# Kernel optimization log

Hardware: AMD Instinct MI355X
Metric: run time of the kernel (lower is better)

The kernel has to match this reference:

```python
import jax, jax.numpy as jnp
import numpy as np

N = 100000
E = 3200000
D = 256
HOPS = 3  # K + 1


def setup_inputs() -> dict:
    key = jax.random.key(0)
    k1, k2, k3, k4, k5 = jax.random.split(key, 5)
    node_features = jax.random.normal(k1, (N, D), dtype=jnp.float32)
    # glorot-uniform-like scale for K+1 Dense kernels
    limit = np.sqrt(6.0 / (D + D)).astype(np.float32)
    W = jax.random.uniform(k2, (HOPS, D, D), dtype=jnp.float32, minval=-limit, maxval=limit)
    adj_vals = jax.random.uniform(k3, (HOPS, E), dtype=jnp.float32)
    adj_rows = jax.random.randint(k4, (HOPS, E), 0, N, dtype=jnp.int32)
    adj_cols = jax.random.randint(k5, (HOPS, E), 0, N, dtype=jnp.int32)
    return {"node_features": node_features, "W": W, "adj_vals": adj_vals,
            "adj_rows": adj_rows, "adj_cols": adj_cols}


def reference(node_features, W, adj_vals, adj_rows, adj_cols):
    """Faithful eval-mode forward: sum over hops of SpMM(A_hop, X @ W_hop), then ReLU.
    Dropout is identity at inference (training=False)."""
    n = node_features.shape[0]
    out = jnp.zeros((n, W.shape[-1]), dtype=node_features.dtype)
    for hop in range(W.shape[0]):  # small fixed K+1 loop, structurally distinct hops
        feats = node_features @ W[hop]                      # [N, out_dim]
        msgs = adj_vals[hop][:, None] * feats[adj_cols[hop]]  # gather + scale, [E, out_dim]
        out = out + jax.ops.segment_sum(msgs, adj_rows[hop], num_segments=n)
    return jax.nn.relu(out)
```

## Files before the change

### kernel.cpp

```cpp
#include <hip/hip_runtime.h>

#define D 256
#define MAXB 128
#define SR 1024
#define PCH 16384

typedef __attribute__((ext_vector_type(8))) short short8;
typedef __attribute__((ext_vector_type(4))) float f32x4;

__device__ __forceinline__ ushort f2b(float f) {
    unsigned u = __float_as_uint(f);
    u += 0x7fffu + ((u >> 16) & 1u);
    return (ushort)(u >> 16);
}
__device__ __forceinline__ float b2f(ushort h) {
    return __uint_as_float(((unsigned)h) << 16);
}
__device__ __forceinline__ long long ntload_ll(const void* p) {
    return __builtin_nontemporal_load((const long long*)p);
}

__global__ void xconv_kernel(const float* __restrict__ X, ushort* __restrict__ Xb, int total8) {
    int i = blockIdx.x * 256 + threadIdx.x;
    if (i >= total8) return;
    const float4 a = *(const float4*)(X + (size_t)i * 8);
    const float4 b = *(const float4*)(X + (size_t)i * 8 + 4);
    ushort o8[8] = {f2b(a.x), f2b(a.y), f2b(a.z), f2b(a.w),
                    f2b(b.x), f2b(b.y), f2b(b.z), f2b(b.w)};
    *(short8*)(Xb + (size_t)i * 8) = *(const short8*)o8;
}

__global__ void wconv_kernel(const float* __restrict__ W, ushort* __restrict__ WT, int total) {
    int idx = blockIdx.x * 256 + threadIdx.x;
    if (idx >= total) return;
    int h = idx >> 16;
    int c = (idx >> 8) & 255, k = idx & 255;
    WT[(h << 16) + c * 256 + k] = f2b(W[(h << 16) + k * 256 + c]);
}

__global__ __launch_bounds__(512) void bpart_kernel(const int* __restrict__ rows,
                                                    const int* __restrict__ cols,
                                                    const float* __restrict__ vals,
                                                    int2* __restrict__ raw,
                                                    int* __restrict__ runofs,
                                                    int e, int nbuk, int nch) {
    __shared__ int lh[MAXB];
    __shared__ int lcur[MAXB];
    int h = blockIdx.y, c = blockIdx.x;
    int c0 = c * PCH, c1 = min(c0 + PCH, e);
    if (c0 >= c1) return;
    const int*   rr = rows + (size_t)h * e;
    const int*   cc = cols + (size_t)h * e;
    const float* vv = vals + (size_t)h * e;
    int tid = threadIdx.x;
    for (int k = tid; k < nbuk; k += 512) { lh[k] = 0; lcur[k] = 0; }
    __syncthreads();
    for (int i = c0 + tid; i < c1; i += 512)
        atomicAdd(&lh[rr[i] >> 10], 1);
    __syncthreads();
    int* ro = runofs + (size_t)(h * nch + c) * (nbuk + 1);
    if (tid == 0) {
        int run = h * e + c0;
        for (int j = 0; j < nbuk; ++j) {
            ro[j] = run;
            int v = lh[j];
            lh[j] = run;
            run += v;
        }
        ro[nbuk] = h * e + c1;
    }
    __syncthreads();
    for (int i = c0 + tid; i < c1; i += 512) {
        int row = rr[i];
        int b = row >> 10;
        int p = lh[b] + atomicAdd(&lcur[b], 1);
        raw[p] = make_int2(cc[i] | ((row & 1023) << 17), __float_as_int(vv[i]));
    }
}

__global__ __launch_bounds__(1024) void bscan_kernel(const int* __restrict__ runofs,
                                                     int* __restrict__ gbase,
                                                     int nbuk, int nch, int nkeytot) {
    __shared__ int s[1024];
    int t = threadIdx.x;
    int sum = 0;
    if (t < nkeytot) {
        int h = t / nbuk, b = t % nbuk;
        for (int c = 0; c < nch; ++c) {
            const int* ro = runofs + (size_t)(h * nch + c) * (nbuk + 1) + b;
            sum += ro[1] - ro[0];
        }
    }
    s[t] = sum;
    __syncthreads();
    for (int off = 1; off < 1024; off <<= 1) {
        int x = (t >= off) ? s[t - off] : 0;
        __syncthreads();
        s[t] += x;
        __syncthreads();
    }
    if (t < nkeytot) gbase[t] = s[t] - sum;
    if (t == nkeytot - 1) gbase[nkeytot] = s[t];
}

__global__ __launch_bounds__(512) void bsort_kernel(const int* __restrict__ gbase,
                                                    const int* __restrict__ runofs,
                                                    const int2* __restrict__ raw,
                                                    int2* __restrict__ eg,
                                                    int* __restrict__ row_ptr,
                                                    int n, int nbuk, int nch) {
    __shared__ int hist[1024];
    __shared__ int ss[512];
    __shared__ int cur[1024];
    int key = blockIdx.x;
    int h = key / nbuk, b = key % nbuk;
    int s = gbase[key], t = gbase[key + 1];
    int tid = threadIdx.x;
    int w = tid >> 6, lane = tid & 63;
    hist[tid] = 0; hist[tid + 512] = 0;
    __syncthreads();
    for (int c = w; c < nch; c += 8) {
        const int* ro = runofs + (size_t)(h * nch + c) * (nbuk + 1) + b;
        int rs = ro[0], re = ro[1];
        for (int i = rs + lane; i < re; i += 64)
            atomicAdd(&hist[(((unsigned)raw[i].x) >> 17) & 1023], 1);
    }
    __syncthreads();
    int a = hist[2 * tid], c2 = hist[2 * tid + 1];
    int pair = a + c2;
    ss[tid] = pair;
    __syncthreads();
    for (int off = 1; off < 512; off <<= 1) {
        int x = (tid >= off) ? ss[tid - off] : 0;
        __syncthreads();
        ss[tid] += x;
        __syncthreads();
    }
    int excl = s + ss[tid] - pair;
    cur[2 * tid] = excl;
    cur[2 * tid + 1] = excl + a;
    int* rp = row_ptr + (size_t)h * (n + 1);
    int grow = b * SR + 2 * tid;
    if (grow < n)     rp[grow]     = excl;
    if (grow + 1 < n) rp[grow + 1] = excl + a;
    if (tid == 0 && b == nbuk - 1) rp[n] = t;
    __syncthreads();
    for (int c = w; c < nch; c += 8) {
        const int* ro = runofs + (size_t)(h * nch + c) * (nbuk + 1) + b;
        int rs = ro[0], re = ro[1];
        for (int i = rs + lane; i < re; i += 64) {
            int2 ev = raw[i];
            int j = (((unsigned)ev.x) >> 17) & 1023;
            int p = atomicAdd(&cur[j], 1);
            eg[p] = ev;
        }
    }
}

__global__ __launch_bounds__(256) void spmmX_kernel(const int* __restrict__ row_ptr,
                                                    const int2* __restrict__ eg,
                                                    const ushort* __restrict__ Xb,
                                                    ushort* __restrict__ Y, int n,
                                                    size_t rpStride, size_t yStride, int half) {
    const int* rp = row_ptr + blockIdx.y * rpStride;
    ushort* Yh = Y + blockIdx.y * yStride;
    int w = threadIdx.x >> 6, lane = threadIdx.x & 63;
    int r = blockIdx.x * 4 + w;
    if (r >= n) return;
    int g = lane >> 4, l4 = lane & 15;
    int doff = half * 128 + l4 * 8;
    const ushort* xb = Xb + doff;
    int e0 = rp[r], e1 = rp[r + 1];
    float acc[8] = {};

    int i0 = e0 + g;
    long long d_cur = (i0 < e1) ? ntload_ll(eg + i0) : 0;
    int c_cur = ((int)(unsigned)d_cur) & 0x1FFFF;
    short8 va = *(const short8*)(xb + (size_t)c_cur * 256);
    int i1 = e0 + 4 + g;
    long long d_nxt = (i1 < e1) ? ntload_ll(eg + i1) : 0;

    for (int ee = e0; ee < e1; ee += 4) {
        int c_nxt = ((int)(unsigned)d_nxt) & 0x1FFFF;
        short8 wa = *(const short8*)(xb + (size_t)c_nxt * 256);
        int i2 = ee + 8 + g;
        long long d_n2 = (i2 < e1) ? ntload_ll(eg + i2) : 0;

        float val = __int_as_float((int)(d_cur >> 32));
        #pragma unroll
        for (int i = 0; i < 8; ++i)
            acc[i] = fmaf(val, b2f((ushort)va[i]), acc[i]);

        d_cur = d_nxt; va = wa; d_nxt = d_n2;
    }
    #pragma unroll
    for (int i = 0; i < 8; ++i) acc[i] += __shfl_xor(acc[i], 16);
    #pragma unroll
    for (int i = 0; i < 8; ++i) acc[i] += __shfl_xor(acc[i], 32);
    if (g == 0) {
        union { ushort u[8]; long long ll[2]; } o;
        #pragma unroll
        for (int i = 0; i < 8; ++i) o.u[i] = f2b(acc[i]);
        long long* dst = (long long*)(Yh + (size_t)r * 256 + doff);
        __builtin_nontemporal_store(o.ll[0], dst);
        __builtin_nontemporal_store(o.ll[1], dst + 1);
    }
}

#define BP 40

__global__ __launch_bounds__(256) void gemmY2_kernel(const ushort* __restrict__ Y,
                                                     const ushort* __restrict__ WT,
                                                     float* __restrict__ out, int M,
                                                     int nh, int hoff, int mode) {
    __shared__ ushort As[64 * BP];
    __shared__ ushort Bs[256 * BP];
    int tid = threadIdx.x;
    int r0 = blockIdx.x * 64;
    int w = tid >> 6, lane = tid & 63;
    int lo = lane & 15, hi = lane >> 4;
    f32x4 acc[16] = {};

    int srow = tid >> 2;
    int skq = (tid & 3) * 8;
    int arow = r0 + srow; if (arow > M - 1) arow = M - 1;

    for (int ks = 0; ks < nh * 8; ++ks) {
        int hh = ks >> 3, k0 = (ks & 7) * 32;
        short8 av = *(const short8*)(Y + ((size_t)hh * M + arow) * 256 + k0 + skq);
        const ushort* bp = WT + ((size_t)(hoff + hh) << 16) + (size_t)tid * 256 + k0;
        short8 bv0 = *(const short8*)(bp);
        short8 bv1 = *(const short8*)(bp + 8);
        short8 bv2 = *(const short8*)(bp + 16);
        short8 bv3 = *(const short8*)(bp + 24);
        __syncthreads();
        *(short8*)&As[srow * BP + skq] = av;
        *(short8*)&Bs[tid * BP +  0] = bv0;
        *(short8*)&Bs[tid * BP +  8] = bv1;
        *(short8*)&Bs[tid * BP + 16] = bv2;
        *(short8*)&Bs[tid * BP + 24] = bv3;
        __syncthreads();
        short8 a = *(const short8*)&As[(w * 16 + lo) * BP + hi * 8];
        #pragma unroll
        for (int j = 0; j < 16; ++j) {
            short8 bf = *(const short8*)&Bs[(j * 16 + lo) * BP + hi * 8];
            acc[j] = __builtin_amdgcn_mfma_f32_16x16x32_bf16(a, bf, acc[j], 0, 0, 0);
        }
    }
    #pragma unroll
    for (int j = 0; j < 16; ++j)
        #pragma unroll
        for (int i = 0; i < 4; ++i) {
            int row = r0 + w * 16 + hi * 4 + i;
            int col = j * 16 + lo;
            if (row < M) {
                float v = acc[j][i];
                float* op = &out[(size_t)row * 256 + col];
                if (mode & 1) v += *op;
                if (mode & 2) v = fmaxf(v, 0.f);
                *op = v;
            }
        }
}

extern "C" void kernel_launch(void* const* d_in, const int* in_sizes, int n_in,
                              void* d_out, int out_size, void* d_ws, size_t ws_size,
                              hipStream_t stream) {
    const float* X    = (const float*)d_in[0];
    const float* W    = (const float*)d_in[1];
    const float* vals = (const float*)d_in[2];
    const int*   rows = (const int*)d_in[3];
    const int*   cols = (const int*)d_in[4];
    int n    = in_sizes[0] / D;
    int hops = in_sizes[1] / (D * D);
    int e    = in_sizes[2] / hops;

    int nbuk    = (n + SR - 1) / SR;
    int nkeytot = hops * nbuk;
    int nch     = (e + PCH - 1) / PCH;

    float* out = (float*)d_out;

    auto padded = [](size_t b) { return (b + 255) & ~(size_t)255; };
    char* wsb = (char*)d_ws;
    size_t off = 0;
    auto alloc = [&](size_t bytes) -> void* { void* p = wsb + off; off += padded(bytes); return p; };

    ushort* WT      = (ushort*)alloc((size_t)hops * D * D * 2);
    ushort* Xb      = (ushort*)alloc((size_t)n * D * 2);
    int*    runofs  = (int*)   alloc((size_t)hops * nch * (nbuk + 1) * 4);
    int*    gbase   = (int*)   alloc((size_t)(nkeytot + 1) * 4);
    int*    row_ptr = (int*)   alloc((size_t)hops * (n + 1) * 4);
    int2*   edges   = (int2*)  alloc((size_t)hops * e * 8);
    size_t  raw_off = off;
    int2*   raw     = (int2*)  alloc((size_t)hops * e * 8);

    bool bigY = (ws_size >= raw_off + (size_t)hops * n * D * 2);
    ushort* Y = (ushort*)raw;

    xconv_kernel<<<(n * D / 8 + 255) / 256, 256, 0, stream>>>(X, Xb, n * D / 8);
    wconv_kernel<<<(hops * D * D + 255) / 256, 256, 0, stream>>>(W, WT, hops * D * D);

    bpart_kernel<<<dim3(nch, hops), 512, 0, stream>>>(rows, cols, vals, raw, runofs, e, nbuk, nch);
    bscan_kernel<<<1, 1024, 0, stream>>>(runofs, gbase, nbuk, nch, nkeytot);
    bsort_kernel<<<nkeytot, 512, 0, stream>>>(gbase, runofs, raw, edges, row_ptr, n, nbuk, nch);

    if (bigY) {
        for (int s = 0; s < 2; ++s)
            spmmX_kernel<<<dim3((n + 3) / 4, hops), 256, 0, stream>>>(row_ptr, edges, Xb, Y, n,
                                                                      (size_t)(n + 1),
                                                                      (size_t)n * D, s);
        gemmY2_kernel<<<(n + 63) / 64, 256, 0, stream>>>(Y, WT, out, n, hops, 0, 2);
    } else {
        for (int h = 0; h < hops; ++h) {
            for (int s = 0; s < 2; ++s)
                spmmX_kernel<<<dim3((n + 3) / 4, 1), 256, 0, stream>>>(row_ptr + (size_t)h * (n + 1),
                                                                       edges, Xb, Y, n, 0, 0, s);
            int mode = (h > 0 ? 1 : 0) | (h == hops - 1 ? 2 : 0);
            gemmY2_kernel<<<(n + 63) / 64, 256, 0, stream>>>(Y, WT, out, n, 1, h, mode);
        }
    }
}
```

Measured before the change: 1.128 ms.

## Per-wave partition histograms, merged hop SpMM launches, and prefetching GEMM loads

The partition kernel now keeps a histogram per wave and derives per-wave scatter bases, which replaces contended shared atomics on a single counter array. The SpMM kernel now handles all hops for a row inside one launch, so the same Xb half-columns are reused while each row is resident. The GEMM register-prefetches the next K-slice of Y and WT while the current slice is in LDS. The bsort histogram pass also reads only the packed column word. The costs are more registers for three accumulator sets and the prefetch, and less grid parallelism in SpMM.

```diff
diff --git a/kernel.cpp b/kernel.cpp
--- a/kernel.cpp
+++ b/kernel.cpp
@@ -44,36 +44,48 @@
                                                     int2* __restrict__ raw,
                                                     int* __restrict__ runofs,
                                                     int e, int nbuk, int nch) {
-    __shared__ int lh[MAXB];
-    __shared__ int lcur[MAXB];
+    __shared__ int whist[8][MAXB];
+    __shared__ int rbase[MAXB];
     int h = blockIdx.y, c = blockIdx.x;
     int c0 = c * PCH, c1 = min(c0 + PCH, e);
     if (c0 >= c1) return;
     const int*   rr = rows + (size_t)h * e;
     const int*   cc = cols + (size_t)h * e;
     const float* vv = vals + (size_t)h * e;
-    int tid = threadIdx.x;
-    for (int k = tid; k < nbuk; k += 512) { lh[k] = 0; lcur[k] = 0; }
+    int tid = threadIdx.x, w = tid >> 6;
+    for (int k = tid; k < 8 * MAXB; k += 512) ((int*)whist)[k] = 0;
     __syncthreads();
     for (int i = c0 + tid; i < c1; i += 512)
-        atomicAdd(&lh[rr[i] >> 10], 1);
+        atomicAdd(&whist[w][rr[i] >> 10], 1);
     __syncthreads();
     int* ro = runofs + (size_t)(h * nch + c) * (nbuk + 1);
     if (tid == 0) {
         int run = h * e + c0;
         for (int j = 0; j < nbuk; ++j) {
             ro[j] = run;
-            int v = lh[j];
-            lh[j] = run;
+            rbase[j] = run;
+            int t = 0;
+            #pragma unroll
+            for (int w2 = 0; w2 < 8; ++w2) t += whist[w2][j];
+            run += t;
+        }
+        ro[nbuk] = h * e + c1;
+    }
+    __syncthreads();
+    if (tid < nbuk) {
+        int run = rbase[tid];
+        #pragma unroll
+        for (int w2 = 0; w2 < 8; ++w2) {
+            int v = whist[w2][tid];
+            whist[w2][tid] = run;
             run += v;
         }
-        ro[nbuk] = h * e + c1;
     }
     __syncthreads();
     for (int i = c0 + tid; i < c1; i += 512) {
         int row = rr[i];
         int b = row >> 10;
-        int p = lh[b] + atomicAdd(&lcur[b], 1);
+        int p = atomicAdd(&whist[w][b], 1);
         raw[p] = make_int2(cc[i] | ((row & 1023) << 17), __float_as_int(vv[i]));
     }
 }
@@ -119,11 +131,12 @@
     int w = tid >> 6, lane = tid & 63;
     hist[tid] = 0; hist[tid + 512] = 0;
     __syncthreads();
+    const int* rawx = (const int*)raw;
     for (int c = w; c < nch; c += 8) {
         const int* ro = runofs + (size_t)(h * nch + c) * (nbuk + 1) + b;
         int rs = ro[0], re = ro[1];
         for (int i = rs + lane; i < re; i += 64)
-            atomicAdd(&hist[(((unsigned)raw[i].x) >> 17) & 1023], 1);
+            atomicAdd(&hist[(((unsigned)rawx[2 * (size_t)i]) >> 17) & 1023], 1);
     }
     __syncthreads();
     int a = hist[2 * tid], c2 = hist[2 * tid + 1];
@@ -161,49 +174,54 @@
                                                     const int2* __restrict__ eg,
                                                     const ushort* __restrict__ Xb,
                                                     ushort* __restrict__ Y, int n,
-                                                    size_t rpStride, size_t yStride, int half) {
-    const int* rp = row_ptr + blockIdx.y * rpStride;
-    ushort* Yh = Y + blockIdx.y * yStride;
+                                                    int nh, size_t rpStride, size_t yStride,
+                                                    int half) {
     int w = threadIdx.x >> 6, lane = threadIdx.x & 63;
     int r = blockIdx.x * 4 + w;
     if (r >= n) return;
     int g = lane >> 4, l4 = lane & 15;
     int doff = half * 128 + l4 * 8;
     const ushort* xb = Xb + doff;
-    int e0 = rp[r], e1 = rp[r + 1];
-    float acc[8] = {};
-
-    int i0 = e0 + g;
-    long long d_cur = (i0 < e1) ? ntload_ll(eg + i0) : 0;
-    int c_cur = ((int)(unsigned)d_cur) & 0x1FFFF;
-    short8 va = *(const short8*)(xb + (size_t)c_cur * 256);
-    int i1 = e0 + 4 + g;
-    long long d_nxt = (i1 < e1) ? ntload_ll(eg + i1) : 0;
-
-    for (int ee = e0; ee < e1; ee += 4) {
-        int c_nxt = ((int)(unsigned)d_nxt) & 0x1FFFF;
-        short8 wa = *(const short8*)(xb + (size_t)c_nxt * 256);
-        int i2 = ee + 8 + g;
-        long long d_n2 = (i2 < e1) ? ntload_ll(eg + i2) : 0;
-
-        float val = __int_as_float((int)(d_cur >> 32));
-        #pragma unroll
-        for (int i = 0; i < 8; ++i)
-            acc[i] = fmaf(val, b2f((ushort)va[i]), acc[i]);
-
-        d_cur = d_nxt; va = wa; d_nxt = d_n2;
-    }
+    float acc[3][8] = {};
+
     #pragma unroll
-    for (int i = 0; i < 8; ++i) acc[i] += __shfl_xor(acc[i], 16);
+    for (int h = 0; h < 3; ++h) {
+        if (h >= nh) break;
+        const int* rp = row_ptr + (size_t)h * rpStride;
+        int e0 = rp[r], e1 = rp[r + 1];
+        int i0 = e0 + g;
+        long long d_cur = (i0 < e1) ? ntload_ll(eg + i0) : 0;
+        int c_cur = ((int)(unsigned)d_cur) & 0x1FFFF;
+        short8 va = *(const short8*)(xb + (size_t)c_cur * 256);
+        int i1 = e0 + 4 + g;
+        long long d_nxt = (i1 < e1) ? ntload_ll(eg + i1) : 0;
+        for (int ee = e0; ee < e1; ee += 4) {
+            int c_nxt = ((int)(unsigned)d_nxt) & 0x1FFFF;
+            short8 wa = *(const short8*)(xb + (size_t)c_nxt * 256);
+            int i2 = ee + 8 + g;
+            long long d_n2 = (i2 < e1) ? ntload_ll(eg + i2) : 0;
+            float val = __int_as_float((int)(d_cur >> 32));
+            #pragma unroll
+            for (int i = 0; i < 8; ++i)
+                acc[h][i] = fmaf(val, b2f((ushort)va[i]), acc[h][i]);
+            d_cur = d_nxt; va = wa; d_nxt = d_n2;
+        }
+    }
     #pragma unroll
-    for (int i = 0; i < 8; ++i) acc[i] += __shfl_xor(acc[i], 32);
-    if (g == 0) {
-        union { ushort u[8]; long long ll[2]; } o;
-        #pragma unroll
-        for (int i = 0; i < 8; ++i) o.u[i] = f2b(acc[i]);
-        long long* dst = (long long*)(Yh + (size_t)r * 256 + doff);
-        __builtin_nontemporal_store(o.ll[0], dst);
-        __builtin_nontemporal_store(o.ll[1], dst + 1);
+    for (int h = 0; h < 3; ++h) {
+        if (h >= nh) break;
+        #pragma unroll
+        for (int i = 0; i < 8; ++i) acc[h][i] += __shfl_xor(acc[h][i], 16);
+        #pragma unroll
+        for (int i = 0; i < 8; ++i) acc[h][i] += __shfl_xor(acc[h][i], 32);
+        if (g == 0) {
+            union { ushort u[8]; long long ll[2]; } o;
+            #pragma unroll
+            for (int i = 0; i < 8; ++i) o.u[i] = f2b(acc[h][i]);
+            long long* dst = (long long*)(Y + (size_t)h * yStride + (size_t)r * 256 + doff);
+            __builtin_nontemporal_store(o.ll[0], dst);
+            __builtin_nontemporal_store(o.ll[1], dst + 1);
+        }
     }
 }
 
@@ -224,21 +242,30 @@
     int srow = tid >> 2;
     int skq = (tid & 3) * 8;
     int arow = r0 + srow; if (arow > M - 1) arow = M - 1;
-
-    for (int ks = 0; ks < nh * 8; ++ks) {
-        int hh = ks >> 3, k0 = (ks & 7) * 32;
-        short8 av = *(const short8*)(Y + ((size_t)hh * M + arow) * 256 + k0 + skq);
-        const ushort* bp = WT + ((size_t)(hoff + hh) << 16) + (size_t)tid * 256 + k0;
-        short8 bv0 = *(const short8*)(bp);
-        short8 bv1 = *(const short8*)(bp + 8);
-        short8 bv2 = *(const short8*)(bp + 16);
-        short8 bv3 = *(const short8*)(bp + 24);
+    int ks_end = nh * 8;
+
+    short8 av = *(const short8*)(Y + (size_t)arow * 256 + skq);
+    const ushort* bp0 = WT + ((size_t)hoff << 16) + (size_t)tid * 256;
+    short8 bv0 = *(const short8*)(bp0);
+    short8 bv1 = *(const short8*)(bp0 + 8);
+    short8 bv2 = *(const short8*)(bp0 + 16);
+    short8 bv3 = *(const short8*)(bp0 + 24);
+
+    for (int ks = 0; ks < ks_end; ++ks) {
         __syncthreads();
         *(short8*)&As[srow * BP + skq] = av;
         *(short8*)&Bs[tid * BP +  0] = bv0;
         *(short8*)&Bs[tid * BP +  8] = bv1;
         *(short8*)&Bs[tid * BP + 16] = bv2;
         *(short8*)&Bs[tid * BP + 24] = bv3;
+        int ks2 = (ks + 1 < ks_end) ? ks + 1 : ks;
+        int hh2 = ks2 >> 3, k02 = (ks2 & 7) * 32;
+        av = *(const short8*)(Y + ((size_t)hh2 * M + arow) * 256 + k02 + skq);
+        const ushort* bp = WT + ((size_t)(hoff + hh2) << 16) + (size_t)tid * 256 + k02;
+        bv0 = *(const short8*)(bp);
+        bv1 = *(const short8*)(bp + 8);
+        bv2 = *(const short8*)(bp + 16);
+        bv3 = *(const short8*)(bp + 24);
         __syncthreads();
         short8 a = *(const short8*)&As[(w * 16 + lo) * BP + hi * 8];
         #pragma unroll
@@ -307,15 +334,14 @@
 
     if (bigY) {
         for (int s = 0; s < 2; ++s)
-            spmmX_kernel<<<dim3((n + 3) / 4, hops), 256, 0, stream>>>(row_ptr, edges, Xb, Y, n,
-                                                                      (size_t)(n + 1),
-                                                                      (size_t)n * D, s);
+            spmmX_kernel<<<(n + 3) / 4, 256, 0, stream>>>(row_ptr, edges, Xb, Y, n, hops,
+                                                          (size_t)(n + 1), (size_t)n * D, s);
         gemmY2_kernel<<<(n + 63) / 64, 256, 0, stream>>>(Y, WT, out, n, hops, 0, 2);
     } else {
         for (int h = 0; h < hops; ++h) {
             for (int s = 0; s < 2; ++s)
-                spmmX_kernel<<<dim3((n + 3) / 4, 1), 256, 0, stream>>>(row_ptr + (size_t)h * (n + 1),
-                                                                       edges, Xb, Y, n, 0, 0, s);
+                spmmX_kernel<<<(n + 3) / 4, 256, 0, stream>>>(row_ptr + (size_t)h * (n + 1),
+                                                              edges, Xb, Y, n, 1, 0, 0, s);
             int mode = (h > 0 ? 1 : 0) | (h == hops - 1 ? 2 : 0);
             gemmY2_kernel<<<(n + 63) / 64, 256, 0, stream>>>(Y, WT, out, n, 1, h, mode);
         }
```

New measurement: 1.190 ms. 1.05x slower.
